# Kernel tuning notes

Hardware: AMD Instinct MI355X
Metric: run time of the kernel (lower is better)

## Reference

```python
import jax, jax.numpy as jnp
import numpy as np

B, N, D, D_MODEL = 4, 2048, 512, 512


def setup_inputs() -> dict:
    key = jax.random.key(0)
    kx, kq, kk, kv, ks = jax.random.split(key, 5)
    scale = 1.0 / np.sqrt(D)
    x = jax.random.normal(kx, (B, N, D), dtype=jnp.float32)
    Wq = (jax.random.normal(kq, (D, D_MODEL), dtype=jnp.float32) * scale)
    Wk = (jax.random.normal(kk, (D, D_MODEL), dtype=jnp.float32) * scale)
    Wv = (jax.random.normal(kv, (D, D_MODEL), dtype=jnp.float32) * scale)
    Ws = (jax.random.normal(ks, (D, 1), dtype=jnp.float32) * scale)
    return {"x": x, "Wq": Wq, "Wk": Wk, "Wv": Wv, "Ws": Ws}


def reference(x, Wq, Wk, Wv, Ws):
    # Projections (Linear, no bias)
    Q = x @ Wq                      # (B, N, d_model)
    K = x @ Wk                      # (B, N, d_model)
    V = x @ Wv                      # (B, N, d_model)
    sigma = x @ Ws                  # (B, N, 1)

    n = x.shape[1]
    dm = Wq.shape[1]

    # Prior association: Gaussian kernel over |i-j| distance, row-normalized
    idx = jnp.arange(n)
    dist = jnp.abs(idx[:, None] - idx[None, :]).astype(x.dtype)      # (N, N)
    inv_norm = 1.0 / (jnp.sqrt(2.0 * jnp.pi).astype(x.dtype) * jnp.abs(sigma))
    gaussian = inv_norm * jnp.exp(-0.5 * jnp.square(dist[None] / sigma))  # (B,N,N)
    P = gaussian / jnp.sum(gaussian, axis=-1, keepdims=True)

    # Series association: scaled dot-product softmax attention
    scores = jnp.einsum('bnd,bmd->bnm', Q, K) / jnp.sqrt(jnp.asarray(dm, x.dtype))
    S = jax.nn.softmax(scores, axis=-1)                               # (B,N,N)

    # Reconstruction
    Z = S @ V                                                          # (B,N,d_model)
    return (Z, P)
```

## Files before the change

kernel.cpp:

```cpp
#include <hip/hip_runtime.h>

typedef float f32x4 __attribute__((ext_vector_type(4)));
typedef short s16x8 __attribute__((ext_vector_type(8)));
typedef unsigned short us4 __attribute__((ext_vector_type(4)));

#define MFMA16(a, b, c) __builtin_amdgcn_mfma_f32_16x16x32_bf16(a, b, c, 0, 0, 0)

#define GLOAD_LDS16(gp, lp) __builtin_amdgcn_global_load_lds( \
    (__attribute__((address_space(1))) void*)(gp),            \
    (__attribute__((address_space(3))) void*)(lp), 16, 0, 0)

__device__ __forceinline__ unsigned short f2bf(float f) {
    union { float f; unsigned u; } v; v.f = f;
    unsigned r = v.u + 0x7fffu + ((v.u >> 16) & 1u);
    return (unsigned short)(r >> 16);
}

#define RP 136
#define SH128 (128 * RP)

__device__ __forceinline__ void gemm_core128(
    const unsigned short* __restrict__ Ab, size_t Astride,
    const unsigned short* __restrict__ Bb, size_t Bstride,
    int K, unsigned short* As, unsigned short* Bs,
    int t, f32x4 acc[4][4])
{
    const int wave = t >> 6, lane = t & 63;
    const int c = lane & 15, quad = lane >> 4;
    const int wm = (wave >> 1) * 64, wn = (wave & 1) * 64;
    const int srow = t >> 2;
    const int scol = (t & 3) * 8;

    for (int k0 = 0; k0 < K; k0 += 32) {
        __syncthreads();
        const unsigned short* ga = Ab + (size_t)srow * Astride + k0 + scol;
        const unsigned short* gb = Bb + (size_t)srow * Bstride + k0 + scol;
        GLOAD_LDS16(ga,                 As + t * 8);
        GLOAD_LDS16(ga + 64 * Astride,  As + 2048 + t * 8);
        GLOAD_LDS16(gb,                 Bs + t * 8);
        GLOAD_LDS16(gb + 64 * Bstride,  Bs + 2048 + t * 8);
        __syncthreads();

        s16x8 af[4], bf[4];
        #pragma unroll
        for (int i = 0; i < 4; i++)
            af[i] = *(const s16x8*)(As + (wm + i * 16 + c) * 32 + quad * 8);
        #pragma unroll
        for (int i = 0; i < 4; i++)
            bf[i] = *(const s16x8*)(Bs + (wn + i * 16 + c) * 32 + quad * 8);
        #pragma unroll
        for (int mt = 0; mt < 4; mt++)
            #pragma unroll
            for (int nt = 0; nt < 4; nt++)
                acc[mt][nt] = MFMA16(af[mt], bf[nt], acc[mt][nt]);
    }
}

__global__ __launch_bounds__(256) void k_convert(
    const float* __restrict__ x, const float* __restrict__ wq,
    const float* __restrict__ wk, const float* __restrict__ wv,
    unsigned short* __restrict__ xbf, unsigned short* __restrict__ wt)
{
    __shared__ __align__(16) unsigned short lt[64][72];

    int bid = blockIdx.x, t = threadIdx.x;
    if (bid < 4096) {
        int gid = bid * 256 + t;
        float4 v = ((const float4*)x)[gid];
        us4 o = { f2bf(v.x), f2bf(v.y), f2bf(v.z), f2bf(v.w) };
        ((us4*)xbf)[gid] = o;
    } else {
        int idx = bid - 4096;
        int w = idx >> 6;
        int tile = idx & 63;
        int tk = tile >> 3, tn = tile & 7;
        const float* src = ((w == 0) ? wq : (w == 1) ? wk : wv)
                         + (size_t)(tk * 64) * 512 + tn * 64;

        int row = t >> 2;
        int c0 = (t & 3) * 16;
        const float4* s = (const float4*)(src + (size_t)row * 512 + c0);
        #pragma unroll
        for (int q = 0; q < 4; q++) {
            float4 v = s[q];
            lt[c0 + q * 4 + 0][row] = f2bf(v.x);
            lt[c0 + q * 4 + 1][row] = f2bf(v.y);
            lt[c0 + q * 4 + 2][row] = f2bf(v.z);
            lt[c0 + q * 4 + 3][row] = f2bf(v.w);
        }
        __syncthreads();

        int n = t >> 2;
        int k0 = (t & 3) * 16;
        s16x8 a = *(const s16x8*)&lt[n][k0];
        s16x8 b = *(const s16x8*)&lt[n][k0 + 8];
        unsigned short* dst = wt + (((size_t)(w * 512 + tn * 64 + n)) << 9)
                                 + tk * 64 + k0;
        *(s16x8*)dst = a;
        *(s16x8*)(dst + 8) = b;
    }
}

__global__ __launch_bounds__(256) void k_proj(
    const unsigned short* __restrict__ xbf, const unsigned short* __restrict__ wt,
    unsigned short* __restrict__ qbf, unsigned short* __restrict__ kbf,
    unsigned short* __restrict__ vtbf)
{
    __shared__ __align__(16) unsigned short sh[SH128];

    int t = threadIdx.x;
    int m0 = blockIdx.x * 128, n0 = blockIdx.y * 128;
    f32x4 acc[4][4] = {};

    gemm_core128(xbf + (size_t)m0 * 512, 512, wt + (size_t)n0 * 512, 512,
                 512, sh, sh + 4096, t, acc);
    __syncthreads();

    int wave = t >> 6, lane = t & 63, c = lane & 15, quad = lane >> 4;
    int wm = (wave >> 1) * 64, wn = (wave & 1) * 64;
    int sel = blockIdx.y >> 2;

    if (sel < 2) {
        unsigned short* dst = sel ? kbf : qbf;
        int ncol0 = n0 - sel * 512;
        #pragma unroll
        for (int mt = 0; mt < 4; mt++)
            #pragma unroll
            for (int nt = 0; nt < 4; nt++)
                #pragma unroll
                for (int r = 0; r < 4; r++)
                    sh[(wm + mt * 16 + quad * 4 + r) * RP + wn + nt * 16 + c]
                        = f2bf(acc[mt][nt][r]);
        __syncthreads();
        int rr = t >> 1, hh = (t & 1) * 64;
        const s16x8* sp = (const s16x8*)(sh + rr * RP + hh);
        s16x8* dp = (s16x8*)(dst + (size_t)(m0 + rr) * 512 + ncol0 + hh);
        s16x8 v[8];
        #pragma unroll
        for (int i = 0; i < 8; i++) v[i] = sp[i];
        #pragma unroll
        for (int i = 0; i < 8; i++) dp[i] = v[i];
    } else {
        #pragma unroll
        for (int mt = 0; mt < 4; mt++)
            #pragma unroll
            for (int nt = 0; nt < 4; nt++)
                #pragma unroll
                for (int r = 0; r < 4; r++)
                    sh[(wn + nt * 16 + c) * RP + wm + mt * 16 + quad * 4 + r]
                        = f2bf(acc[mt][nt][r]);
        __syncthreads();
        int bb = m0 >> 11, nn0 = m0 & 2047;
        int dbase = n0 - 1024;
        int dl = t >> 1, nh = (t & 1) * 64;
        const s16x8* sp = (const s16x8*)(sh + dl * RP + nh);
        s16x8* dp = (s16x8*)(vtbf + ((size_t)(bb * 512 + dbase + dl)) * 2048
                                  + nn0 + nh);
        s16x8 v[8];
        #pragma unroll
        for (int i = 0; i < 8; i++) v[i] = sp[i];
        #pragma unroll
        for (int i = 0; i < 8; i++) dp[i] = v[i];
    }
}

__device__ __forceinline__ void score_body(
    const unsigned short* __restrict__ qbf, const unsigned short* __restrict__ kbf,
    unsigned short* __restrict__ pbf,
    int b, int m0, int n0, int t, unsigned short* sh)
{
    f32x4 acc[4][4] = {};
    gemm_core128(qbf + (size_t)(b * 2048 + m0) * 512, 512,
                 kbf + (size_t)(b * 2048 + n0) * 512, 512,
                 512, sh, sh + 4096, t, acc);
    __syncthreads();

    int wave = t >> 6, lane = t & 63, c = lane & 15, quad = lane >> 4;
    int wm = (wave >> 1) * 64, wn = (wave & 1) * 64;
    const float scale = 0.044194173824159216f;

    #pragma unroll
    for (int mt = 0; mt < 4; mt++) {
        #pragma unroll
        for (int r = 0; r < 4; r++) {
            int row = wm + mt * 16 + quad * 4 + r;
            #pragma unroll
            for (int nt = 0; nt < 4; nt++) {
                float p = __expf(acc[mt][nt][r] * scale);
                sh[row * RP + wn + nt * 16 + c] = f2bf(p);
            }
        }
    }
    __syncthreads();
    int rr = t >> 1, hh = (t & 1) * 64;
    const s16x8* sp = (const s16x8*)(sh + rr * RP + hh);
    s16x8* dp = (s16x8*)(pbf + (size_t)(b * 2048 + m0 + rr) * 2048 + n0 + hh);
    s16x8 v[8];
    #pragma unroll
    for (int i = 0; i < 8; i++) v[i] = sp[i];
    #pragma unroll
    for (int i = 0; i < 8; i++) dp[i] = v[i];
}

__device__ __forceinline__ void prior_wave(
    const float* __restrict__ x, const float* __restrict__ wsv,
    float* __restrict__ pout, int row, int lane)
{
    const float4* xr = (const float4*)(x + (size_t)row * 512);
    const float4* wr = (const float4*)wsv;
    float4 a0 = xr[lane * 2],     b0 = wr[lane * 2];
    float4 a1 = xr[lane * 2 + 1], b1 = wr[lane * 2 + 1];
    float part = a0.x * b0.x + a0.y * b0.y + a0.z * b0.z + a0.w * b0.w
               + a1.x * b1.x + a1.y * b1.y + a1.z * b1.z + a1.w * b1.w;
    #pragma unroll
    for (int o = 32; o; o >>= 1) part += __shfl_xor(part, o, 64);
    float sigma = part;
    float inv2 = 0.5f / (sigma * sigma);

    int i = row & 2047;
    float g[32];
    float sum = 0.f;
    #pragma unroll
    for (int u = 0; u < 8; u++) {
        #pragma unroll
        for (int v = 0; v < 4; v++) {
            float d = (float)(u * 256 + lane * 4 + v - i);
            float e = __expf(-(d * d) * inv2);
            g[u * 4 + v] = e;
            sum += e;
        }
    }
    #pragma unroll
    for (int o = 32; o; o >>= 1) sum += __shfl_xor(sum, o, 64);
    float inv = 1.0f / sum;

    float4* pr = (float4*)(pout + (size_t)row * 2048);
    #pragma unroll
    for (int u = 0; u < 8; u++) {
        float4 o4 = { g[u * 4] * inv, g[u * 4 + 1] * inv,
                      g[u * 4 + 2] * inv, g[u * 4 + 3] * inv };
        pr[u * 64 + lane] = o4;
    }
}

__global__ __launch_bounds__(256) void k_score_prior(
    const unsigned short* __restrict__ qbf, const unsigned short* __restrict__ kbf,
    unsigned short* __restrict__ pbf,
    const float* __restrict__ x, const float* __restrict__ wsv,
    float* __restrict__ pout)
{
    __shared__ __align__(16) unsigned short sh[SH128];

    int bid = blockIdx.x, t = threadIdx.x;
    if (bid < 1024) {
        int b = bid >> 8, r = bid & 255;
        score_body(qbf, kbf, pbf, b, (r & 15) * 128, (r >> 4) * 128, t, sh);
    } else {
        int row = (bid - 1024) * 4 + (t >> 6);
        prior_wave(x, wsv, pout, row, t & 63);
    }
}

__global__ __launch_bounds__(256) void k_score(
    const unsigned short* __restrict__ qbf, const unsigned short* __restrict__ kbf,
    unsigned short* __restrict__ pbf)
{
    __shared__ __align__(16) unsigned short sh[SH128];
    score_body(qbf, kbf, pbf, blockIdx.z,
               blockIdx.x * 128, blockIdx.y * 128, threadIdx.x, sh);
}

__global__ __launch_bounds__(256) void k_out(
    const unsigned short* __restrict__ pbf, const unsigned short* __restrict__ vtbf,
    float* __restrict__ zout)
{
    __shared__ __align__(16) unsigned short As[128 * 32];
    __shared__ __align__(16) unsigned short Bs[64 * 32];

    int t = threadIdx.x;
    int b = blockIdx.z;
    int m0 = blockIdx.x * 128, n0 = blockIdx.y * 64;

    const int wave = t >> 6, lane = t & 63;
    const int c = lane & 15, quad = lane >> 4;
    const int wm = (wave >> 1) * 64, wn = (wave & 1) * 32;
    const int srow = t >> 2;
    const int scol = (t & 3) * 8;

    const unsigned short* Ab = pbf + (size_t)(b * 2048 + m0) * 2048;
    const unsigned short* Bb = vtbf + (size_t)(b * 512 + n0) * 2048;

    s16x8 ones;
    #pragma unroll
    for (int i = 0; i < 8; i++) ones[i] = (short)0x3F80;

    f32x4 acc[4][2] = {};
    f32x4 accl[4] = {};

    for (int k0 = 0; k0 < 2048; k0 += 32) {
        __syncthreads();
        const unsigned short* ga = Ab + (size_t)srow * 2048 + k0 + scol;
        GLOAD_LDS16(ga,             As + t * 8);
        GLOAD_LDS16(ga + 64 * 2048, As + 2048 + t * 8);
        GLOAD_LDS16(Bb + (size_t)srow * 2048 + k0 + scol, Bs + t * 8);
        __syncthreads();

        s16x8 af[4], bf[2];
        #pragma unroll
        for (int i = 0; i < 4; i++)
            af[i] = *(const s16x8*)(As + (wm + i * 16 + c) * 32 + quad * 8);
        #pragma unroll
        for (int i = 0; i < 2; i++)
            bf[i] = *(const s16x8*)(Bs + (wn + i * 16 + c) * 32 + quad * 8);
        #pragma unroll
        for (int mt = 0; mt < 4; mt++) {
            #pragma unroll
            for (int nt = 0; nt < 2; nt++)
                acc[mt][nt] = MFMA16(af[mt], bf[nt], acc[mt][nt]);
            accl[mt] = MFMA16(af[mt], ones, accl[mt]);
        }
    }

    #pragma unroll
    for (int mt = 0; mt < 4; mt++) {
        #pragma unroll
        for (int r = 0; r < 4; r++) {
            int row = wm + mt * 16 + quad * 4 + r;
            float inv = 1.0f / accl[mt][r];
            #pragma unroll
            for (int nt = 0; nt < 2; nt++) {
                zout[(size_t)(b * 2048 + m0 + row) * 512 + n0 + wn + nt * 16 + c]
                    = acc[mt][nt][r] * inv;
            }
        }
    }
}

__global__ __launch_bounds__(256) void k_prior(
    const float* __restrict__ x, const float* __restrict__ wsv,
    float* __restrict__ pout)
{
    int row = blockIdx.x * 4 + (threadIdx.x >> 6);
    prior_wave(x, wsv, pout, row, threadIdx.x & 63);
}

extern "C" void kernel_launch(void* const* d_in, const int* in_sizes, int n_in,
                              void* d_out, int out_size, void* d_ws, size_t ws_size,
                              hipStream_t stream)
{
    const float* x  = (const float*)d_in[0];
    const float* wq = (const float*)d_in[1];
    const float* wk = (const float*)d_in[2];
    const float* wv = (const float*)d_in[3];
    const float* ws = (const float*)d_in[4];

    float* zout = (float*)d_out;
    float* pout = zout + (size_t)4 * 2048 * 512;

    const size_t need = ((size_t)4194304 + 786432 + 3 * 4194304 + 16777216) * 2;

    if (ws_size >= need) {
        unsigned short* base = (unsigned short*)d_ws;
        unsigned short* xbf  = base;
        unsigned short* wt   = xbf  + (size_t)4194304;
        unsigned short* qbf  = wt   + (size_t)786432;
        unsigned short* kbf  = qbf  + (size_t)4194304;
        unsigned short* vtbf = kbf  + (size_t)4194304;
        unsigned short* pbf  = vtbf + (size_t)4194304;

        k_convert<<<dim3(4288), dim3(256), 0, stream>>>(x, wq, wk, wv, xbf, wt);
        k_proj       <<<dim3(64, 12),   dim3(256), 0, stream>>>(xbf, wt, qbf, kbf, vtbf);
        k_score_prior<<<dim3(3072),     dim3(256), 0, stream>>>(qbf, kbf, pbf, x, ws, pout);
        k_out        <<<dim3(16, 8, 4), dim3(256), 0, stream>>>(pbf, vtbf, zout);
    } else {
        unsigned short* base = (unsigned short*)pout;
        unsigned short* pbf  = base;
        unsigned short* qbf  = base + (size_t)16777216;
        unsigned short* kbf  = qbf  + (size_t)4194304;
        unsigned short* vtbf = kbf  + (size_t)4194304;
        unsigned short* xbf  = base;
        unsigned short* wt   = base + (size_t)4194304;

        k_convert<<<dim3(4288), dim3(256), 0, stream>>>(x, wq, wk, wv, xbf, wt);
        k_proj  <<<dim3(64, 12),    dim3(256), 0, stream>>>(xbf, wt, qbf, kbf, vtbf);
        k_score <<<dim3(16, 16, 4), dim3(256), 0, stream>>>(qbf, kbf, pbf);
        k_out   <<<dim3(16, 8, 4),  dim3(256), 0, stream>>>(pbf, vtbf, zout);
        k_prior <<<dim3(2048),      dim3(256), 0, stream>>>(x, ws, pout);
    }
}
```

Measured before the change: 206.4 us.

## Double-buffer LDS tiles in the GEMM main loops to overlap loads with MFMA

Converts the shared GEMM core (used by the projection and score kernels) and the P·V output kernel to a two-stage LDS ping-pong. The next K-slice is issued with global_load_lds into the alternate buffer before the current slice is read and multiplied, and only one barrier per iteration remains instead of two. The aim is to hide global-to-LDS latency behind MFMA work. In exchange it uses more LDS in k_out. The overlap may also be lost if the compiler inserts a full vmcnt wait before the LDS reads.

```diff
diff --git a/kernel.cpp b/kernel.cpp
--- a/kernel.cpp
+++ b/kernel.cpp
@@ -19,11 +19,10 @@
 #define RP 136
 #define SH128 (128 * RP)
 
-__device__ __forceinline__ void gemm_core128(
+__device__ __forceinline__ void gemm_core128_db(
     const unsigned short* __restrict__ Ab, size_t Astride,
     const unsigned short* __restrict__ Bb, size_t Bstride,
-    int K, unsigned short* As, unsigned short* Bs,
-    int t, f32x4 acc[4][4])
+    int K, unsigned short* sh, int t, f32x4 acc[4][4])
 {
     const int wave = t >> 6, lane = t & 63;
     const int c = lane & 15, quad = lane >> 4;
@@ -31,28 +30,39 @@
     const int srow = t >> 2;
     const int scol = (t & 3) * 8;
 
+    const unsigned short* ga = Ab + (size_t)srow * Astride + scol;
+    const unsigned short* gb = Bb + (size_t)srow * Bstride + scol;
+
+    GLOAD_LDS16(ga,                 sh + t * 8);
+    GLOAD_LDS16(ga + 64 * Astride,  sh + 2048 + t * 8);
+    GLOAD_LDS16(gb,                 sh + 4096 + t * 8);
+    GLOAD_LDS16(gb + 64 * Bstride,  sh + 4096 + 2048 + t * 8);
+    __syncthreads();
+
+    int cur = 0;
     for (int k0 = 0; k0 < K; k0 += 32) {
-        __syncthreads();
-        const unsigned short* ga = Ab + (size_t)srow * Astride + k0 + scol;
-        const unsigned short* gb = Bb + (size_t)srow * Bstride + k0 + scol;
-        GLOAD_LDS16(ga,                 As + t * 8);
-        GLOAD_LDS16(ga + 64 * Astride,  As + 2048 + t * 8);
-        GLOAD_LDS16(gb,                 Bs + t * 8);
-        GLOAD_LDS16(gb + 64 * Bstride,  Bs + 2048 + t * 8);
-        __syncthreads();
-
+        const unsigned short* buf = sh + cur * 8192;
+        if (k0 + 32 < K) {
+            unsigned short* nb = sh + (cur ^ 1) * 8192;
+            GLOAD_LDS16(ga + k0 + 32,                 nb + t * 8);
+            GLOAD_LDS16(ga + k0 + 32 + 64 * Astride,  nb + 2048 + t * 8);
+            GLOAD_LDS16(gb + k0 + 32,                 nb + 4096 + t * 8);
+            GLOAD_LDS16(gb + k0 + 32 + 64 * Bstride,  nb + 4096 + 2048 + t * 8);
+        }
         s16x8 af[4], bf[4];
         #pragma unroll
         for (int i = 0; i < 4; i++)
-            af[i] = *(const s16x8*)(As + (wm + i * 16 + c) * 32 + quad * 8);
+            af[i] = *(const s16x8*)(buf + (wm + i * 16 + c) * 32 + quad * 8);
         #pragma unroll
         for (int i = 0; i < 4; i++)
-            bf[i] = *(const s16x8*)(Bs + (wn + i * 16 + c) * 32 + quad * 8);
+            bf[i] = *(const s16x8*)(buf + 4096 + (wn + i * 16 + c) * 32 + quad * 8);
         #pragma unroll
         for (int mt = 0; mt < 4; mt++)
             #pragma unroll
             for (int nt = 0; nt < 4; nt++)
                 acc[mt][nt] = MFMA16(af[mt], bf[nt], acc[mt][nt]);
+        __syncthreads();
+        cur ^= 1;
     }
 }
 
@@ -112,9 +122,8 @@
     int m0 = blockIdx.x * 128, n0 = blockIdx.y * 128;
     f32x4 acc[4][4] = {};
 
-    gemm_core128(xbf + (size_t)m0 * 512, 512, wt + (size_t)n0 * 512, 512,
-                 512, sh, sh + 4096, t, acc);
-    __syncthreads();
+    gemm_core128_db(xbf + (size_t)m0 * 512, 512, wt + (size_t)n0 * 512, 512,
+                    512, sh, t, acc);
 
     int wave = t >> 6, lane = t & 63, c = lane & 15, quad = lane >> 4;
     int wm = (wave >> 1) * 64, wn = (wave & 1) * 64;
@@ -170,10 +179,9 @@
     int b, int m0, int n0, int t, unsigned short* sh)
 {
     f32x4 acc[4][4] = {};
-    gemm_core128(qbf + (size_t)(b * 2048 + m0) * 512, 512,
-                 kbf + (size_t)(b * 2048 + n0) * 512, 512,
-                 512, sh, sh + 4096, t, acc);
-    __syncthreads();
+    gemm_core128_db(qbf + (size_t)(b * 2048 + m0) * 512, 512,
+                    kbf + (size_t)(b * 2048 + n0) * 512, 512,
+                    512, sh, t, acc);
 
     int wave = t >> 6, lane = t & 63, c = lane & 15, quad = lane >> 4;
     int wm = (wave >> 1) * 64, wn = (wave & 1) * 64;
@@ -274,8 +282,7 @@
     const unsigned short* __restrict__ pbf, const unsigned short* __restrict__ vtbf,
     float* __restrict__ zout)
 {
-    __shared__ __align__(16) unsigned short As[128 * 32];
-    __shared__ __align__(16) unsigned short Bs[64 * 32];
+    __shared__ __align__(16) unsigned short sh[12288];
 
     int t = threadIdx.x;
     int b = blockIdx.z;
@@ -287,8 +294,8 @@
     const int srow = t >> 2;
     const int scol = (t & 3) * 8;
 
-    const unsigned short* Ab = pbf + (size_t)(b * 2048 + m0) * 2048;
-    const unsigned short* Bb = vtbf + (size_t)(b * 512 + n0) * 2048;
+    const unsigned short* ga = pbf + (size_t)(b * 2048 + m0 + srow) * 2048 + scol;
+    const unsigned short* gb = vtbf + (size_t)(b * 512 + n0 + srow) * 2048 + scol;
 
     s16x8 ones;
     #pragma unroll
@@ -297,21 +304,27 @@
     f32x4 acc[4][2] = {};
     f32x4 accl[4] = {};
 
+    GLOAD_LDS16(ga,             sh + t * 8);
+    GLOAD_LDS16(ga + 64 * 2048, sh + 2048 + t * 8);
+    GLOAD_LDS16(gb,             sh + 4096 + t * 8);
+    __syncthreads();
+
+    int cur = 0;
     for (int k0 = 0; k0 < 2048; k0 += 32) {
-        __syncthreads();
-        const unsigned short* ga = Ab + (size_t)srow * 2048 + k0 + scol;
-        GLOAD_LDS16(ga,             As + t * 8);
-        GLOAD_LDS16(ga + 64 * 2048, As + 2048 + t * 8);
-        GLOAD_LDS16(Bb + (size_t)srow * 2048 + k0 + scol, Bs + t * 8);
-        __syncthreads();
-
+        const unsigned short* buf = sh + cur * 6144;
+        if (k0 + 32 < 2048) {
+            unsigned short* nb = sh + (cur ^ 1) * 6144;
+            GLOAD_LDS16(ga + k0 + 32,             nb + t * 8);
+            GLOAD_LDS16(ga + k0 + 32 + 64 * 2048, nb + 2048 + t * 8);
+            GLOAD_LDS16(gb + k0 + 32,             nb + 4096 + t * 8);
+        }
         s16x8 af[4], bf[2];
         #pragma unroll
         for (int i = 0; i < 4; i++)
-            af[i] = *(const s16x8*)(As + (wm + i * 16 + c) * 32 + quad * 8);
+            af[i] = *(const s16x8*)(buf + (wm + i * 16 + c) * 32 + quad * 8);
         #pragma unroll
         for (int i = 0; i < 2; i++)
-            bf[i] = *(const s16x8*)(Bs + (wn + i * 16 + c) * 32 + quad * 8);
+            bf[i] = *(const s16x8*)(buf + 4096 + (wn + i * 16 + c) * 32 + quad * 8);
         #pragma unroll
         for (int mt = 0; mt < 4; mt++) {
             #pragma unroll
@@ -319,6 +332,8 @@
                 acc[mt][nt] = MFMA16(af[mt], bf[nt], acc[mt][nt]);
             accl[mt] = MFMA16(af[mt], ones, accl[mt]);
         }
+        __syncthreads();
+        cur ^= 1;
     }
 
     #pragma unroll
```

Measured after the change: 199.1 us. 3.5% less time.
